# Kernel optimization log

Hardware: AMD Instinct MI355X
Metric: run time of the kernel (lower is better)

The kernel has to match this reference:

```python
import jax, jax.numpy as jnp
import numpy as np

N = 50000
NEG_SLOPE = 0.2  # PyG GATConv default negative_slope


def gat_conv(x, src, dst, W, a_src, a_dst, b, heads, out_dim, concat):
    # x: [N, F_in]; W: [F_in, heads*out_dim]; a_src/a_dst: [heads, out_dim]
    h = (x @ W).reshape(N, heads, out_dim)                      # [N,H,D]
    alpha_src = jnp.einsum('nhd,hd->nh', h, a_src)              # [N,H]
    alpha_dst = jnp.einsum('nhd,hd->nh', h, a_dst)              # [N,H]
    e = jax.nn.leaky_relu(alpha_src[src] + alpha_dst[dst], NEG_SLOPE)  # [E,H]
    # segment softmax over incoming edges of each destination node
    m = jax.ops.segment_max(e, dst, num_segments=N)             # [N,H]
    ex = jnp.exp(e - m[dst])
    denom = jax.ops.segment_sum(ex, dst, num_segments=N)        # [N,H]
    alpha = ex / (denom[dst] + 1e-16)                           # [E,H]
    msg = h[src] * alpha[:, :, None]                            # [E,H,D]
    out = jax.ops.segment_sum(msg, dst, num_segments=N)         # [N,H,D]
    out = out.reshape(N, heads * out_dim) if concat else out.mean(axis=1)
    return out + b


def setup_inputs() -> dict:
    key = jax.random.key(0)
    ks = jax.random.split(key, 14)
    E = 800000
    IN, HID, H, LAT = 128, 64, 4, 64

    def glorot(k, shape):
        fan = shape[0] + shape[-1]
        return jax.random.uniform(k, shape, jnp.float32, -1.0, 1.0) * np.sqrt(6.0 / fan)

    return {
        'x': jax.random.normal(ks[0], (N, IN), jnp.float32),
        'edge_index': jax.random.randint(ks[1], (2, E), 0, N, jnp.int64),
        'W1': glorot(ks[2], (IN, H * HID)),
        'a_src1': glorot(ks[3], (H, HID)),
        'a_dst1': glorot(ks[4], (H, HID)),
        'b1': jnp.zeros((H * HID,), jnp.float32),
        'W_mu': glorot(ks[5], (H * HID, LAT)),
        'a_src_mu': glorot(ks[6], (1, LAT)),
        'a_dst_mu': glorot(ks[7], (1, LAT)),
        'b_mu': jnp.zeros((LAT,), jnp.float32),
        'W_ls': glorot(ks[8], (H * HID, LAT)),
        'a_src_ls': glorot(ks[9], (1, LAT)),
        'a_dst_ls': glorot(ks[10], (1, LAT)),
        'b_ls': jnp.zeros((LAT,), jnp.float32),
    }


def reference(x, edge_index, W1, a_src1, a_dst1, b1,
              W_mu, a_src_mu, a_dst_mu, b_mu,
              W_ls, a_src_ls, a_dst_ls, b_ls):
    # PyG GATConv adds self-loops by default
    loops = jnp.arange(N, dtype=edge_index.dtype)
    src = jnp.concatenate([edge_index[0], loops])
    dst = jnp.concatenate([edge_index[1], loops])

    h = jax.nn.relu(gat_conv(x, src, dst, W1, a_src1, a_dst1, b1, 4, 64, True))
    mu = gat_conv(h, src, dst, W_mu, a_src_mu, a_dst_mu, b_mu, 1, 64, False)
    logstd = gat_conv(h, src, dst, W_ls, a_src_ls, a_dst_ls, b_ls, 1, 64, False)
    return (mu, logstd)
```

## Files before the change

### kernel.cpp

```cpp
#include <hip/hip_runtime.h>
#include <hip/hip_bf16.h>

#define NNODES 50000
#define MT 3125
#define NB 196
typedef __hip_bfloat16 bf16;
typedef __attribute__((ext_vector_type(8))) short bf16x8;
typedef __attribute__((ext_vector_type(4))) float f32x4;

__device__ __forceinline__ void unpack2(unsigned w, float& lo, float& hi){
  lo = __uint_as_float(w << 16);
  hi = __uint_as_float(w & 0xffff0000u);
}
__device__ __forceinline__ short f2bf(float f){
  union { __hip_bfloat16 h; short s; } u; u.h = __float2bfloat16(f); return u.s;
}
__device__ __forceinline__ float lrelu(float v){ return v > 0.f ? v : 0.2f * v; }

__global__ __launch_bounds__(256)
void cvt_w_k(const float* __restrict__ W1, const float* __restrict__ Wmu,
             const float* __restrict__ Wls, bf16x8* __restrict__ Bp1,
             bf16x8* __restrict__ Bp2){
  int t = blockIdx.x * 256 + threadIdx.x;
  if (t < 4096){
    int lane = t & 63, ct = (t >> 6) & 15, kt = t >> 10;
    int k0 = kt * 32 + (lane >> 4) * 8, col = ct * 16 + (lane & 15);
    bf16x8 o;
    #pragma unroll
    for (int j = 0; j < 8; j++) o[j] = f2bf(W1[(size_t)(k0 + j) * 256 + col]);
    Bp1[t] = o;
  } else if (t < 8192){
    int u = t - 4096;
    int lane = u & 63, ct = (u >> 6) & 7, kt = u >> 9;
    int k0 = kt * 32 + (lane >> 4) * 8, col = ct * 16 + (lane & 15);
    const float* W = (col < 64) ? Wmu : Wls;
    int cc = col & 63;
    bf16x8 o;
    #pragma unroll
    for (int j = 0; j < 8; j++) o[j] = f2bf(W[(size_t)(k0 + j) * 64 + cc]);
    Bp2[u] = o;
  }
}

__global__ __launch_bounds__(256)
void gemm1_mfma(const float* __restrict__ x, const bf16x8* __restrict__ Bp,
                const float* __restrict__ aS, const float* __restrict__ aD,
                bf16* __restrict__ Y, float* __restrict__ as1, float* __restrict__ ad1){
  int rt = blockIdx.x;
  int w = threadIdx.x >> 6, lane = threadIdx.x & 63;
  const float* xr = x + (size_t)(rt * 16 + (lane & 15)) * 128 + (lane >> 4) * 8;
  f32x4 z = {0.f, 0.f, 0.f, 0.f};
  f32x4 acc[4] = {z, z, z, z};
  for (int kt = 0; kt < 4; kt++){
    float4 v0 = *(const float4*)(xr + kt * 32);
    float4 v1 = *(const float4*)(xr + kt * 32 + 4);
    bf16x8 a;
    a[0] = f2bf(v0.x); a[1] = f2bf(v0.y); a[2] = f2bf(v0.z); a[3] = f2bf(v0.w);
    a[4] = f2bf(v1.x); a[5] = f2bf(v1.y); a[6] = f2bf(v1.z); a[7] = f2bf(v1.w);
    #pragma unroll
    for (int c = 0; c < 4; c++){
      bf16x8 b = Bp[(size_t)(kt * 16 + w * 4 + c) * 64 + lane];
      acc[c] = __builtin_amdgcn_mfma_f32_16x16x32_bf16(a, b, acc[c], 0, 0, 0);
    }
  }
  int row0 = rt * 16 + (lane >> 4) * 4;
  #pragma unroll
  for (int c = 0; c < 4; c++){
    int col = w * 64 + c * 16 + (lane & 15);
    #pragma unroll
    for (int i = 0; i < 4; i++)
      Y[(size_t)(row0 + i) * 256 + col] = __float2bfloat16(acc[c][i]);
  }
  float aSv[4], aDv[4];
  #pragma unroll
  for (int c = 0; c < 4; c++){
    int col = c * 16 + (lane & 15);
    aSv[c] = aS[w * 64 + col];
    aDv[c] = aD[w * 64 + col];
  }
  #pragma unroll
  for (int i = 0; i < 4; i++){
    float s1 = 0.f, s2 = 0.f;
    #pragma unroll
    for (int c = 0; c < 4; c++){
      s1 = fmaf(acc[c][i], aSv[c], s1);
      s2 = fmaf(acc[c][i], aDv[c], s2);
    }
    #pragma unroll
    for (int o = 1; o < 16; o <<= 1){
      s1 += __shfl_xor(s1, o);
      s2 += __shfl_xor(s2, o);
    }
    if ((lane & 15) == 0){
      int node = row0 + i;
      as1[node * 4 + w] = s1;
      ad1[node * 4 + w] = s2;
    }
  }
}

__global__ __launch_bounds__(256)
void gemm2_mfma(const bf16x8* __restrict__ Ap, const bf16x8* __restrict__ Bp,
                const float* __restrict__ aSmu, const float* __restrict__ aDmu,
                const float* __restrict__ aSls, const float* __restrict__ aDls,
                bf16* __restrict__ Y2,
                float* __restrict__ as2m, float* __restrict__ ad2m,
                float* __restrict__ as2l, float* __restrict__ ad2l){
  int w = threadIdx.x >> 6, lane = threadIdx.x & 63;
  int rt = blockIdx.x * 4 + w;
  if (rt >= MT) return;
  f32x4 z = {0.f, 0.f, 0.f, 0.f};
  f32x4 acc[8] = {z, z, z, z, z, z, z, z};
  for (int kt = 0; kt < 8; kt++){
    bf16x8 a = Ap[(size_t)(rt * 8 + kt) * 64 + lane];
    #pragma unroll
    for (int c = 0; c < 8; c++){
      bf16x8 b = Bp[(size_t)(kt * 8 + c) * 64 + lane];
      acc[c] = __builtin_amdgcn_mfma_f32_16x16x32_bf16(a, b, acc[c], 0, 0, 0);
    }
  }
  int row0 = rt * 16 + (lane >> 4) * 4;
  #pragma unroll
  for (int c = 0; c < 4; c++){
    int col = c * 16 + (lane & 15);
    #pragma unroll
    for (int i = 0; i < 4; i++){
      Y2[(size_t)(row0 + i) * 128 + col]       = __float2bfloat16(acc[c][i]);
      Y2[(size_t)(row0 + i) * 128 + 64 + col]  = __float2bfloat16(acc[4 + c][i]);
    }
  }
  float aSm[4], aDm[4], aSl[4], aDl[4];
  #pragma unroll
  for (int c = 0; c < 4; c++){
    int col = c * 16 + (lane & 15);
    aSm[c] = aSmu[col]; aDm[c] = aDmu[col];
    aSl[c] = aSls[col]; aDl[c] = aDls[col];
  }
  #pragma unroll
  for (int i = 0; i < 4; i++){
    float s1 = 0.f, s2 = 0.f, s3 = 0.f, s4 = 0.f;
    #pragma unroll
    for (int c = 0; c < 4; c++){
      s1 = fmaf(acc[c][i], aSm[c], s1);
      s2 = fmaf(acc[c][i], aDm[c], s2);
      s3 = fmaf(acc[4 + c][i], aSl[c], s3);
      s4 = fmaf(acc[4 + c][i], aDl[c], s4);
    }
    #pragma unroll
    for (int o = 1; o < 16; o <<= 1){
      s1 += __shfl_xor(s1, o);
      s2 += __shfl_xor(s2, o);
      s3 += __shfl_xor(s3, o);
      s4 += __shfl_xor(s4, o);
    }
    if ((lane & 15) == 0){
      int node = row0 + i;
      as2m[node] = s1; ad2m[node] = s2;
      as2l[node] = s3; ad2l[node] = s4;
    }
  }
}

__global__ __launch_bounds__(256)
void bhist_k(const int* __restrict__ ei, int E0, int Etot, int* __restrict__ bcnt){
  __shared__ int lh[NB];
  for (int i = threadIdx.x; i < NB; i += 256) lh[i] = 0;
  __syncthreads();
  int base = blockIdx.x * 1024 + threadIdx.x;
  #pragma unroll
  for (int q = 0; q < 4; q++){
    int e = base + q * 256;
    if (e < Etot){
      int d = (e < E0) ? ei[E0 + e] : e - E0;
      atomicAdd(&lh[d >> 8], 1);
    }
  }
  __syncthreads();
  for (int i = threadIdx.x; i < NB; i += 256)
    if (lh[i]) atomicAdd(&bcnt[i], lh[i]);
}

__global__ __launch_bounds__(256)
void bscan_k(const int* __restrict__ bcnt, int* __restrict__ bbase,
             int* __restrict__ bcur, int total){
  __shared__ int buf[256];
  int t = threadIdx.x;
  int v = (t < NB) ? bcnt[t] : 0;
  buf[t] = v; __syncthreads();
  int acc = v;
  for (int off = 1; off < 256; off <<= 1){
    int x = (t >= off) ? buf[t - off] : 0;
    __syncthreads();
    acc += x; buf[t] = acc; __syncthreads();
  }
  if (t < NB){ int ex = acc - v; bbase[t] = ex; bcur[t] = ex; }
  if (t == 0) bbase[NB] = total;
}

__global__ __launch_bounds__(256)
void bscat_k(const int* __restrict__ ei, int E0, int Etot,
             int* __restrict__ bcur, unsigned* __restrict__ buck){
  __shared__ int lh[NB];
  __shared__ int lbase[NB];
  for (int i = threadIdx.x; i < NB; i += 256) lh[i] = 0;
  __syncthreads();
  int base = blockIdx.x * 1024 + threadIdx.x;
  int sA[4], dA[4], rA[4];
  #pragma unroll
  for (int q = 0; q < 4; q++){
    int e = base + q * 256;
    sA[q] = -1;
    if (e < Etot){
      int s, d;
      if (e < E0){ s = ei[e]; d = ei[E0 + e]; } else { s = d = e - E0; }
      sA[q] = s; dA[q] = d;
      rA[q] = atomicAdd(&lh[d >> 8], 1);
    }
  }
  __syncthreads();
  for (int i = threadIdx.x; i < NB; i += 256)
    lbase[i] = lh[i] ? atomicAdd(&bcur[i], lh[i]) : 0;
  __syncthreads();
  #pragma unroll
  for (int q = 0; q < 4; q++){
    if (sA[q] >= 0){
      int bk = dA[q] >> 8;
      buck[lbase[bk] + rA[q]] = ((unsigned)(dA[q] & 255) << 16) | (unsigned)sA[q];
    }
  }
}

__global__ __launch_bounds__(256)
void bcsr_k(const unsigned* __restrict__ buck, const int* __restrict__ bbase,
            int* __restrict__ offs, int* __restrict__ srcs, int n){
  int b = blockIdx.x;
  int lo = bbase[b], hi = bbase[b + 1];
  __shared__ int eh[256];
  __shared__ int buf[256];
  int t = threadIdx.x;
  eh[t] = 0;
  __syncthreads();
  for (int j = lo + t; j < hi; j += 256)
    atomicAdd(&eh[(buck[j] >> 16) & 255], 1);
  __syncthreads();
  int v = eh[t];
  buf[t] = v; __syncthreads();
  int acc = v;
  for (int off = 1; off < 256; off <<= 1){
    int x = (t >= off) ? buf[t - off] : 0;
    __syncthreads();
    acc += x; buf[t] = acc; __syncthreads();
  }
  int loff = acc - v;
  int node = b * 256 + t;
  if (node < n) offs[node] = lo + loff;
  if (b == NB - 1 && t == 0) offs[n] = bbase[NB];
  __syncthreads();
  eh[t] = loff;
  __syncthreads();
  for (int j = lo + t; j < hi; j += 256){
    unsigned val = buck[j];
    int dlo = (val >> 16) & 255;
    int rank = atomicAdd(&eh[dlo], 1);
    srcs[lo + rank] = (int)(val & 0xffffu);
  }
}

__global__ __launch_bounds__(128)
void gat_aggr1_k(const int* __restrict__ offs, const int* __restrict__ srcs,
                 const float* __restrict__ as, const float* __restrict__ ad,
                 const bf16* __restrict__ h, const float* __restrict__ b,
                 bf16x8* __restrict__ Ap2, int n){
  int node = blockIdx.x * 2 + (threadIdx.x >> 6);
  if (node >= n) return;
  int lane = threadIdx.x & 63;
  int beg = offs[node], end = offs[node + 1];
  int hA = lane >> 4, iA = lane & 15;
  float advA = ad[node * 4 + hA];
  float m = -1e30f;
  for (int j = beg + iA; j < end; j += 16)
    m = fmaxf(m, lrelu(as[srcs[j] * 4 + hA] + advA));
  #pragma unroll
  for (int o = 1; o < 16; o <<= 1) m = fmaxf(m, __shfl_xor(m, o));
  int hP = (lane >> 3) & 3, oct = lane & 7, slot = lane >> 5;
  float mP   = __shfl(m, hP * 16);
  float advP = __shfl(advA, hP * 16);
  float s = 0.f;
  float acc[8];
  #pragma unroll
  for (int i = 0; i < 8; i++) acc[i] = 0.f;
  #pragma unroll 8
  for (int j0 = beg; j0 < end; j0 += 2){
    int j = j0 + slot;
    if (j < end){
      int si = srcs[j];
      float e = lrelu(as[si * 4 + hP] + advP);
      float p = __expf(e - mP);
      s += p;
      uint4 dw = *(const uint4*)(h + (size_t)si * 256 + hP * 64 + oct * 8);
      float lo, hi;
      unpack2(dw.x, lo, hi); acc[0] = fmaf(lo, p, acc[0]); acc[1] = fmaf(hi, p, acc[1]);
      unpack2(dw.y, lo, hi); acc[2] = fmaf(lo, p, acc[2]); acc[3] = fmaf(hi, p, acc[3]);
      unpack2(dw.z, lo, hi); acc[4] = fmaf(lo, p, acc[4]); acc[5] = fmaf(hi, p, acc[5]);
      unpack2(dw.w, lo, hi); acc[6] = fmaf(lo, p, acc[6]); acc[7] = fmaf(hi, p, acc[7]);
    }
  }
  s += __shfl_xor(s, 32);
  #pragma unroll
  for (int i = 0; i < 8; i++) acc[i] += __shfl_xor(acc[i], 32);
  if (lane < 32){
    float inv = 1.f / (s + 1e-16f);
    bf16x8 o;
    #pragma unroll
    for (int i = 0; i < 8; i++){
      float vv = acc[i] * inv + b[lane * 8 + i];
      o[i] = f2bf(vv > 0.f ? vv : 0.f);
    }
    int kt = lane >> 2, g = lane & 3;
    int rt = node >> 4, r = node & 15;
    Ap2[(size_t)(rt * 8 + kt) * 64 + g * 16 + r] = o;
  }
}

__global__ __launch_bounds__(128)
void gat_aggr2_k(const int* __restrict__ offs, const int* __restrict__ srcs,
                 const float* __restrict__ as2m, const float* __restrict__ ad2m,
                 const float* __restrict__ as2l, const float* __restrict__ ad2l,
                 const bf16* __restrict__ h2,
                 const float* __restrict__ bmu, const float* __restrict__ bls,
                 float* __restrict__ outmu, float* __restrict__ outls, int n){
  int node = blockIdx.x * 2 + (threadIdx.x >> 6);
  if (node >= n) return;
  int lane = threadIdx.x & 63;
  int beg = offs[node], end = offs[node + 1];
  const float* asA = (lane >= 32) ? as2l : as2m;
  float advA = ((lane >= 32) ? ad2l : ad2m)[node];
  int iA = lane & 31;
  float m = -1e30f;
  for (int j = beg + iA; j < end; j += 32)
    m = fmaxf(m, lrelu(asA[srcs[j]] + advA));
  #pragma unroll
  for (int o = 1; o < 32; o <<= 1) m = fmaxf(m, __shfl_xor(m, o));
  int br = (lane >> 3) & 1, oct = lane & 7, slot = lane >> 4;
  float mP   = __shfl(m, br * 32);
  float advP = __shfl(advA, br * 32);
  const float* asP = br ? as2l : as2m;
  float s = 0.f;
  float acc[8];
  #pragma unroll
  for (int i = 0; i < 8; i++) acc[i] = 0.f;
  #pragma unroll 8
  for (int j0 = beg; j0 < end; j0 += 4){
    int j = j0 + slot;
    if (j < end){
      int si = srcs[j];
      float e = lrelu(asP[si] + advP);
      float p = __expf(e - mP);
      s += p;
      uint4 dw = *(const uint4*)(h2 + (size_t)si * 128 + br * 64 + oct * 8);
      float lo, hi;
      unpack2(dw.x, lo, hi); acc[0] = fmaf(lo, p, acc[0]); acc[1] = fmaf(hi, p, acc[1]);
      unpack2(dw.y, lo, hi); acc[2] = fmaf(lo, p, acc[2]); acc[3] = fmaf(hi, p, acc[3]);
      unpack2(dw.z, lo, hi); acc[4] = fmaf(lo, p, acc[4]); acc[5] = fmaf(hi, p, acc[5]);
      unpack2(dw.w, lo, hi); acc[6] = fmaf(lo, p, acc[6]); acc[7] = fmaf(hi, p, acc[7]);
    }
  }
  #pragma unroll
  for (int off = 16; off <= 32; off <<= 1){
    s += __shfl_xor(s, off);
    #pragma unroll
    for (int i = 0; i < 8; i++) acc[i] += __shfl_xor(acc[i], off);
  }
  if (lane < 16){
    float inv = 1.f / (s + 1e-16f);
    const float* bb = (lane >= 8) ? bls : bmu;
    float* out = (lane >= 8) ? outls : outmu;
    float v[8];
    #pragma unroll
    for (int i = 0; i < 8; i++) v[i] = acc[i] * inv + bb[oct * 8 + i];
    float* op = out + (size_t)node * 64 + oct * 8;
    *(float4*)op       = make_float4(v[0], v[1], v[2], v[3]);
    *(float4*)(op + 4) = make_float4(v[4], v[5], v[6], v[7]);
  }
}

extern "C" void kernel_launch(void* const* d_in, const int* in_sizes, int n_in,
                              void* d_out, int out_size, void* d_ws, size_t ws_size,
                              hipStream_t stream){
  const float* x    = (const float*)d_in[0];
  const int*   ei   = (const int*)d_in[1];
  const float* W1   = (const float*)d_in[2];
  const float* aS1  = (const float*)d_in[3];
  const float* aD1  = (const float*)d_in[4];
  const float* b1   = (const float*)d_in[5];
  const float* Wmu  = (const float*)d_in[6];
  const float* aSmu = (const float*)d_in[7];
  const float* aDmu = (const float*)d_in[8];
  const float* bmu  = (const float*)d_in[9];
  const float* Wls  = (const float*)d_in[10];
  const float* aSls = (const float*)d_in[11];
  const float* aDls = (const float*)d_in[12];
  const float* bls  = (const float*)d_in[13];

  const int N    = NNODES;
  const int E0   = in_sizes[1] / 2;
  const int Etot = E0 + N;

  float* ws = (float*)d_ws;
  bf16x8* Ap2  = (bf16x8*)(ws);
  bf16*   h1bf = (bf16*)(ws + 6400000);
  bf16*   h2   = (bf16*)(ws + 12800000);
  float*  as1  = ws + 16000000;
  float*  ad1  = ws + 16200000;
  float*  as2m = ws + 16400000;
  float*  ad2m = ws + 16450000;
  float*  as2l = ws + 16500000;
  float*  ad2l = ws + 16550000;
  int*      offs  = (int*)(ws + 16600000);
  int*      srcs  = (int*)(ws + 16650016);
  unsigned* buck  = (unsigned*)(ws + 17500016);
  int*      bcnt  = (int*)(ws + 18350016);
  int*      bbase = (int*)(ws + 18350272);
  int*      bcur  = (int*)(ws + 18350544);
  bf16x8*   Bp1   = (bf16x8*)(ws + 18351040);
  bf16x8*   Bp2   = (bf16x8*)(ws + 18367424);

  float* outmu = (float*)d_out;
  float* outls = (float*)d_out + 3200000;

  const int egrid4 = (Etot + 1023) / 1024;

  hipMemsetAsync(bcnt, 0, 256 * sizeof(int), stream);
  bhist_k<<<egrid4, 256, 0, stream>>>(ei, E0, Etot, bcnt);
  bscan_k<<<1, 256, 0, stream>>>(bcnt, bbase, bcur, Etot);
  bscat_k<<<egrid4, 256, 0, stream>>>(ei, E0, Etot, bcur, buck);
  bcsr_k<<<NB, 256, 0, stream>>>(buck, bbase, offs, srcs, N);

  cvt_w_k<<<32, 256, 0, stream>>>(W1, Wmu, Wls, Bp1, Bp2);

  gemm1_mfma<<<MT, 256, 0, stream>>>(x, Bp1, aS1, aD1, h1bf, as1, ad1);
  gat_aggr1_k<<<(N + 1) / 2, 128, 0, stream>>>(offs, srcs, as1, ad1, h1bf, b1, Ap2, N);

  gemm2_mfma<<<(MT + 3) / 4, 256, 0, stream>>>(Ap2, Bp2, aSmu, aDmu, aSls, aDls,
                                               h2, as2m, ad2m, as2l, ad2l);
  gat_aggr2_k<<<(N + 1) / 2, 128, 0, stream>>>(offs, srcs, as2m, ad2m, as2l, ad2l,
                                               h2, bmu, bls, outmu, outls, N);
}
```

Measured before the change: 230.9 us.

## Drop histogram pass via fixed-capacity bucket slabs; make aggregation loops branchless

```diff
diff --git a/kernel.cpp b/kernel.cpp
--- a/kernel.cpp
+++ b/kernel.cpp
@@ -4,6 +4,7 @@
 #define NNODES 50000
 #define MT 3125
 #define NB 196
+#define BCAP 5248
 typedef __hip_bfloat16 bf16;
 typedef __attribute__((ext_vector_type(8))) short bf16x8;
 typedef __attribute__((ext_vector_type(4))) float f32x4;
@@ -162,27 +163,41 @@
 }
 
 __global__ __launch_bounds__(256)
-void bhist_k(const int* __restrict__ ei, int E0, int Etot, int* __restrict__ bcnt){
+void bscat_k(const int* __restrict__ ei, int E0, int Etot,
+             int* __restrict__ bcnt, unsigned* __restrict__ buck){
   __shared__ int lh[NB];
+  __shared__ int lbase[NB];
   for (int i = threadIdx.x; i < NB; i += 256) lh[i] = 0;
   __syncthreads();
   int base = blockIdx.x * 1024 + threadIdx.x;
+  int sA[4], dA[4], rA[4];
   #pragma unroll
   for (int q = 0; q < 4; q++){
     int e = base + q * 256;
+    sA[q] = -1;
     if (e < Etot){
-      int d = (e < E0) ? ei[E0 + e] : e - E0;
-      atomicAdd(&lh[d >> 8], 1);
+      int s, d;
+      if (e < E0){ s = ei[e]; d = ei[E0 + e]; } else { s = d = e - E0; }
+      sA[q] = s; dA[q] = d;
+      rA[q] = atomicAdd(&lh[d >> 8], 1);
     }
   }
   __syncthreads();
   for (int i = threadIdx.x; i < NB; i += 256)
-    if (lh[i]) atomicAdd(&bcnt[i], lh[i]);
-}
-
-__global__ __launch_bounds__(256)
-void bscan_k(const int* __restrict__ bcnt, int* __restrict__ bbase,
-             int* __restrict__ bcur, int total){
+    lbase[i] = lh[i] ? atomicAdd(&bcnt[i], lh[i]) : 0;
+  __syncthreads();
+  #pragma unroll
+  for (int q = 0; q < 4; q++){
+    if (sA[q] >= 0){
+      int bk = dA[q] >> 8;
+      buck[(size_t)bk * BCAP + lbase[bk] + rA[q]] =
+          ((unsigned)(dA[q] & 255) << 16) | (unsigned)sA[q];
+    }
+  }
+}
+
+__global__ __launch_bounds__(256)
+void bscan_k(const int* __restrict__ bcnt, int* __restrict__ bbase, int total){
   __shared__ int buf[256];
   int t = threadIdx.x;
   int v = (t < NB) ? bcnt[t] : 0;
@@ -193,55 +208,25 @@
     __syncthreads();
     acc += x; buf[t] = acc; __syncthreads();
   }
-  if (t < NB){ int ex = acc - v; bbase[t] = ex; bcur[t] = ex; }
+  if (t < NB) bbase[t] = acc - v;
   if (t == 0) bbase[NB] = total;
 }
 
 __global__ __launch_bounds__(256)
-void bscat_k(const int* __restrict__ ei, int E0, int Etot,
-             int* __restrict__ bcur, unsigned* __restrict__ buck){
-  __shared__ int lh[NB];
-  __shared__ int lbase[NB];
-  for (int i = threadIdx.x; i < NB; i += 256) lh[i] = 0;
-  __syncthreads();
-  int base = blockIdx.x * 1024 + threadIdx.x;
-  int sA[4], dA[4], rA[4];
-  #pragma unroll
-  for (int q = 0; q < 4; q++){
-    int e = base + q * 256;
-    sA[q] = -1;
-    if (e < Etot){
-      int s, d;
-      if (e < E0){ s = ei[e]; d = ei[E0 + e]; } else { s = d = e - E0; }
-      sA[q] = s; dA[q] = d;
-      rA[q] = atomicAdd(&lh[d >> 8], 1);
-    }
-  }
-  __syncthreads();
-  for (int i = threadIdx.x; i < NB; i += 256)
-    lbase[i] = lh[i] ? atomicAdd(&bcur[i], lh[i]) : 0;
-  __syncthreads();
-  #pragma unroll
-  for (int q = 0; q < 4; q++){
-    if (sA[q] >= 0){
-      int bk = dA[q] >> 8;
-      buck[lbase[bk] + rA[q]] = ((unsigned)(dA[q] & 255) << 16) | (unsigned)sA[q];
-    }
-  }
-}
-
-__global__ __launch_bounds__(256)
-void bcsr_k(const unsigned* __restrict__ buck, const int* __restrict__ bbase,
+void bcsr_k(const unsigned* __restrict__ buck, const int* __restrict__ bcnt,
+            const int* __restrict__ bbase,
             int* __restrict__ offs, int* __restrict__ srcs, int n){
   int b = blockIdx.x;
-  int lo = bbase[b], hi = bbase[b + 1];
+  int cntb = bcnt[b];
+  int gbase = bbase[b];
+  const unsigned* slab = buck + (size_t)b * BCAP;
   __shared__ int eh[256];
   __shared__ int buf[256];
   int t = threadIdx.x;
   eh[t] = 0;
   __syncthreads();
-  for (int j = lo + t; j < hi; j += 256)
-    atomicAdd(&eh[(buck[j] >> 16) & 255], 1);
+  for (int j = t; j < cntb; j += 256)
+    atomicAdd(&eh[(slab[j] >> 16) & 255], 1);
   __syncthreads();
   int v = eh[t];
   buf[t] = v; __syncthreads();
@@ -253,20 +238,20 @@
   }
   int loff = acc - v;
   int node = b * 256 + t;
-  if (node < n) offs[node] = lo + loff;
+  if (node < n) offs[node] = gbase + loff;
   if (b == NB - 1 && t == 0) offs[n] = bbase[NB];
   __syncthreads();
   eh[t] = loff;
   __syncthreads();
-  for (int j = lo + t; j < hi; j += 256){
-    unsigned val = buck[j];
+  for (int j = t; j < cntb; j += 256){
+    unsigned val = slab[j];
     int dlo = (val >> 16) & 255;
     int rank = atomicAdd(&eh[dlo], 1);
-    srcs[lo + rank] = (int)(val & 0xffffu);
-  }
-}
-
-__global__ __launch_bounds__(128)
+    srcs[gbase + rank] = (int)(val & 0xffffu);
+  }
+}
+
+__global__ __launch_bounds__(128, 8)
 void gat_aggr1_k(const int* __restrict__ offs, const int* __restrict__ srcs,
                  const float* __restrict__ as, const float* __restrict__ ad,
                  const bf16* __restrict__ h, const float* __restrict__ b,
@@ -292,18 +277,18 @@
   #pragma unroll 8
   for (int j0 = beg; j0 < end; j0 += 2){
     int j = j0 + slot;
-    if (j < end){
-      int si = srcs[j];
-      float e = lrelu(as[si * 4 + hP] + advP);
-      float p = __expf(e - mP);
-      s += p;
-      uint4 dw = *(const uint4*)(h + (size_t)si * 256 + hP * 64 + oct * 8);
-      float lo, hi;
-      unpack2(dw.x, lo, hi); acc[0] = fmaf(lo, p, acc[0]); acc[1] = fmaf(hi, p, acc[1]);
-      unpack2(dw.y, lo, hi); acc[2] = fmaf(lo, p, acc[2]); acc[3] = fmaf(hi, p, acc[3]);
-      unpack2(dw.z, lo, hi); acc[4] = fmaf(lo, p, acc[4]); acc[5] = fmaf(hi, p, acc[5]);
-      unpack2(dw.w, lo, hi); acc[6] = fmaf(lo, p, acc[6]); acc[7] = fmaf(hi, p, acc[7]);
-    }
+    bool val = j < end;
+    int jc = val ? j : end - 1;
+    int si = srcs[jc];
+    float e = lrelu(as[si * 4 + hP] + advP);
+    float p = val ? __expf(e - mP) : 0.f;
+    s += p;
+    uint4 dw = *(const uint4*)(h + (size_t)si * 256 + hP * 64 + oct * 8);
+    float lo, hi;
+    unpack2(dw.x, lo, hi); acc[0] = fmaf(lo, p, acc[0]); acc[1] = fmaf(hi, p, acc[1]);
+    unpack2(dw.y, lo, hi); acc[2] = fmaf(lo, p, acc[2]); acc[3] = fmaf(hi, p, acc[3]);
+    unpack2(dw.z, lo, hi); acc[4] = fmaf(lo, p, acc[4]); acc[5] = fmaf(hi, p, acc[5]);
+    unpack2(dw.w, lo, hi); acc[6] = fmaf(lo, p, acc[6]); acc[7] = fmaf(hi, p, acc[7]);
   }
   s += __shfl_xor(s, 32);
   #pragma unroll
@@ -322,7 +307,7 @@
   }
 }
 
-__global__ __launch_bounds__(128)
+__global__ __launch_bounds__(128, 8)
 void gat_aggr2_k(const int* __restrict__ offs, const int* __restrict__ srcs,
                  const float* __restrict__ as2m, const float* __restrict__ ad2m,
                  const float* __restrict__ as2l, const float* __restrict__ ad2l,
@@ -352,18 +337,18 @@
   #pragma unroll 8
   for (int j0 = beg; j0 < end; j0 += 4){
     int j = j0 + slot;
-    if (j < end){
-      int si = srcs[j];
-      float e = lrelu(asP[si] + advP);
-      float p = __expf(e - mP);
-      s += p;
-      uint4 dw = *(const uint4*)(h2 + (size_t)si * 128 + br * 64 + oct * 8);
-      float lo, hi;
-      unpack2(dw.x, lo, hi); acc[0] = fmaf(lo, p, acc[0]); acc[1] = fmaf(hi, p, acc[1]);
-      unpack2(dw.y, lo, hi); acc[2] = fmaf(lo, p, acc[2]); acc[3] = fmaf(hi, p, acc[3]);
-      unpack2(dw.z, lo, hi); acc[4] = fmaf(lo, p, acc[4]); acc[5] = fmaf(hi, p, acc[5]);
-      unpack2(dw.w, lo, hi); acc[6] = fmaf(lo, p, acc[6]); acc[7] = fmaf(hi, p, acc[7]);
-    }
+    bool val = j < end;
+    int jc = val ? j : end - 1;
+    int si = srcs[jc];
+    float e = lrelu(asP[si] + advP);
+    float p = val ? __expf(e - mP) : 0.f;
+    s += p;
+    uint4 dw = *(const uint4*)(h2 + (size_t)si * 128 + br * 64 + oct * 8);
+    float lo, hi;
+    unpack2(dw.x, lo, hi); acc[0] = fmaf(lo, p, acc[0]); acc[1] = fmaf(hi, p, acc[1]);
+    unpack2(dw.y, lo, hi); acc[2] = fmaf(lo, p, acc[2]); acc[3] = fmaf(hi, p, acc[3]);
+    unpack2(dw.z, lo, hi); acc[4] = fmaf(lo, p, acc[4]); acc[5] = fmaf(hi, p, acc[5]);
+    unpack2(dw.w, lo, hi); acc[6] = fmaf(lo, p, acc[6]); acc[7] = fmaf(hi, p, acc[7]);
   }
   #pragma unroll
   for (int off = 16; off <= 32; off <<= 1){
@@ -419,11 +404,10 @@
   int*      offs  = (int*)(ws + 16600000);
   int*      srcs  = (int*)(ws + 16650016);
   unsigned* buck  = (unsigned*)(ws + 17500016);
-  int*      bcnt  = (int*)(ws + 18350016);
-  int*      bbase = (int*)(ws + 18350272);
-  int*      bcur  = (int*)(ws + 18350544);
-  bf16x8*   Bp1   = (bf16x8*)(ws + 18351040);
-  bf16x8*   Bp2   = (bf16x8*)(ws + 18367424);
+  int*      bcnt  = (int*)(ws + 18528640);
+  int*      bbase = (int*)(ws + 18528896);
+  bf16x8*   Bp1   = (bf16x8*)(ws + 18529200);
+  bf16x8*   Bp2   = (bf16x8*)(ws + 18545584);
 
   float* outmu = (float*)d_out;
   float* outls = (float*)d_out + 3200000;
@@ -431,10 +415,9 @@
   const int egrid4 = (Etot + 1023) / 1024;
 
   hipMemsetAsync(bcnt, 0, 256 * sizeof(int), stream);
-  bhist_k<<<egrid4, 256, 0, stream>>>(ei, E0, Etot, bcnt);
-  bscan_k<<<1, 256, 0, stream>>>(bcnt, bbase, bcur, Etot);
-  bscat_k<<<egrid4, 256, 0, stream>>>(ei, E0, Etot, bcur, buck);
-  bcsr_k<<<NB, 256, 0, stream>>>(buck, bbase, offs, srcs, N);
+  bscat_k<<<egrid4, 256, 0, stream>>>(ei, E0, Etot, bcnt, buck);
+  bscan_k<<<1, 256, 0, stream>>>(bcnt, bbase, Etot);
+  bcsr_k<<<NB, 256, 0, stream>>>(buck, bcnt, bbase, offs, srcs, N);
 
   cvt_w_k<<<32, 256, 0, stream>>>(W1, Wmu, Wls, Bp1, Bp2);
 
```

Result: faster. 219.8 us (-4.8%).
